# Optimization experiments

Hardware: AMD Instinct MI355X
Metric: run time of the kernel (lower is better)

## Reference

```python
import jax, jax.numpy as jnp
import numpy as np
from jax import lax

ITERATIONS = 10
B, I, D, J, E = 512, 7, 512, 64, 128


def setup_inputs() -> dict:
    key = jax.random.key(0)
    k1, k2, k3 = jax.random.split(key, 3)
    f_bid = jax.random.normal(k1, (B, I, D), dtype=jnp.float32)
    p_bi = jax.random.uniform(k2, (B, I), dtype=jnp.float32)
    weights = jax.random.normal(k3, (I, D, J, E), dtype=jnp.float32)
    return {"f_bid": f_bid, "p_bi": p_bi, "weights": weights}


def reference(f_bid, p_bi, weights):
    # Precompute the per-capsule vote tensor once: [B, I, J, E]
    f_W_bije = jnp.einsum('bid,idje->bije', f_bid, weights)
    b = f_bid.shape[0]
    j, e = weights.shape[2], weights.shape[3]
    c0 = jnp.ones((b, j, e), dtype=f_bid.dtype)

    def body(c_bj, _):
        # routing logits over output capsules j, softmax over j (dim=-1 of 'bij')
        r_bij = jax.nn.softmax(jnp.einsum('bije,bje->bij', f_W_bije, c_bj), axis=-1)
        c_next = jnp.einsum('bi,bij,bije->bje', p_bi, r_bij, f_W_bije)
        return c_next, r_bij

    c_bj, r_stack = lax.scan(body, c0, None, length=ITERATIONS)
    return c_bj, r_stack[-1]
```

## Files before the change

### kernel.cpp

```cpp
#include <hip/hip_runtime.h>
#include <hip/hip_bf16.h>

#define B_SZ 512
#define I_SZ 7
#define D_SZ 512
#define J_SZ 64
#define E_SZ 128
#define N_SZ 8192
#define ITERS 10

typedef __attribute__((ext_vector_type(8))) short bf16x8;
typedef __attribute__((ext_vector_type(4))) float f32x4;

#if defined(__has_builtin)
#if __has_builtin(__builtin_amdgcn_cvt_pk_bf16_f32)
#define HAVE_CVT_PK_BF16 1
#endif
#endif

__device__ inline void split2(float x0, float x1, unsigned& hp, unsigned& lp) {
#ifdef HAVE_CVT_PK_BF16
    auto h = __builtin_amdgcn_cvt_pk_bf16_f32(x0, x1);
    hp = __builtin_bit_cast(unsigned, h);
    union { unsigned u; float f; } b0, b1;
    b0.u = hp << 16;
    b1.u = hp & 0xFFFF0000u;
    auto l = __builtin_amdgcn_cvt_pk_bf16_f32(x0 - b0.f, x1 - b1.f);
    lp = __builtin_bit_cast(unsigned, l);
#else
    union { float f; unsigned u; } u0, u1;
    u0.f = x0; u1.f = x1;
    unsigned r0 = u0.u + 0x7FFF + ((u0.u >> 16) & 1);
    unsigned r1 = u1.u + 0x7FFF + ((u1.u >> 16) & 1);
    hp = __builtin_amdgcn_perm(r1, r0, 0x07060302);
    union { unsigned u; float f; } h0, h1;
    h0.u = r0 & 0xFFFF0000u;
    h1.u = r1 & 0xFFFF0000u;
    union { float f; unsigned u; } s0, s1;
    s0.f = x0 - h0.f; s1.f = x1 - h1.f;
    unsigned q0 = s0.u + 0x7FFF + ((s0.u >> 16) & 1);
    unsigned q1 = s1.u + 0x7FFF + ((s1.u >> 16) & 1);
    lp = __builtin_amdgcn_perm(q1, q0, 0x07060302);
#endif
}

__device__ inline void gload16(const float* g, float* l) {
    __builtin_amdgcn_global_load_lds(
        (const __attribute__((address_space(1))) void*)g,
        (__attribute__((address_space(3))) void*)l, 16, 0, 0);
}

__global__ __launch_bounds__(512) void vote_gemm_mfma(
    const float* __restrict__ f,
    const float* __restrict__ W,
    float* __restrict__ fW)
{
    const int i  = blockIdx.z;
    const int m0 = blockIdx.y * 256;
    const int n0 = blockIdx.x * 256;
    const int th = threadIdx.x;
    const int lane = th & 63;
    const int wave = th >> 6;
    const int wr  = wave >> 2;
    const int wc  = wave & 3;
    const int q   = lane >> 4;
    const int l15 = lane & 15;

    __shared__ float ldsA[2][256 * 32];
    __shared__ float ldsB[2][32 * 256];

    const float* aSrc[4];
    const float* bSrc[4];
#pragma unroll
    for (int ci = 0; ci < 4; ++ci) {
        const int ia = ci * 512 + th;
        const int mA = ia >> 3, sA = ia & 7;
        aSrc[ci] = f + (size_t)(m0 + mA) * (I_SZ * D_SZ) + (size_t)i * D_SZ
                     + ((sA ^ (mA & 7)) << 2);
        const int ib = ci * 512 + th;
        const int kB = ib >> 6, cB = ib & 63;
        bSrc[ci] = W + (size_t)i * D_SZ * N_SZ + (size_t)kB * N_SZ + n0
                     + ((cB ^ ((kB & 8) >> 1)) << 2);
    }

    auto stage = [&](int slot) {
#pragma unroll
        for (int ci = 0; ci < 4; ++ci)
            gload16(aSrc[ci], &ldsA[slot][(ci * 512 + th) * 4]);
#pragma unroll
        for (int ci = 0; ci < 4; ++ci)
            gload16(bSrc[ci], &ldsB[slot][(ci * 512 + th) * 4]);
#pragma unroll
        for (int ci = 0; ci < 4; ++ci) {
            aSrc[ci] += 32;
            bSrc[ci] += (size_t)32 * N_SZ;
        }
    };

    f32x4 acc[8][4];
#pragma unroll
    for (int a = 0; a < 8; ++a)
#pragma unroll
        for (int c = 0; c < 4; ++c)
            acc[a][c] = (f32x4){0.f, 0.f, 0.f, 0.f};

    stage(0);
    stage(1);
    asm volatile("s_waitcnt vmcnt(8)" ::: "memory");
    __builtin_amdgcn_s_barrier();
    asm volatile("" ::: "memory");

    for (int t = 0; t < 16; ++t) {
        const int slot = t & 1;
        const float* Ab = &ldsA[slot][0];
        const float* Bb = &ldsB[slot][0];

        uint4 Bh4[4], Bl4[4];
#pragma unroll
        for (int ns = 0; ns < 4; ++ns) {
            const int cs = (wc * 16 + ns * 4 + (l15 >> 2)) ^ ((q & 1) << 2);
            const float* bp = Bb + q * 8 * 256 + cs * 4 + (l15 & 3);
            const float b0 = bp[0 * 256], b1 = bp[1 * 256], b2 = bp[2 * 256], b3 = bp[3 * 256];
            const float b4 = bp[4 * 256], b5 = bp[5 * 256], b6 = bp[6 * 256], b7 = bp[7 * 256];
            split2(b0, b1, Bh4[ns].x, Bl4[ns].x);
            split2(b2, b3, Bh4[ns].y, Bl4[ns].y);
            split2(b4, b5, Bh4[ns].z, Bl4[ns].z);
            split2(b6, b7, Bh4[ns].w, Bl4[ns].w);
        }

#pragma unroll
        for (int ms = 0; ms < 8; ++ms) {
            const int mrow = wr * 128 + ms * 16 + l15;
            const int p0 = (q * 2) ^ (l15 & 7);
            const float4 va = *(const float4*)(Ab + mrow * 32 + ((p0 ^ 0) << 2));
            const float4 vb = *(const float4*)(Ab + mrow * 32 + ((p0 ^ 1) << 2));
            uint4 ah, al;
            split2(va.x, va.y, ah.x, al.x);
            split2(va.z, va.w, ah.y, al.y);
            split2(vb.x, vb.y, ah.z, al.z);
            split2(vb.z, vb.w, ah.w, al.w);
            const bf16x8 Ah = __builtin_bit_cast(bf16x8, ah);
            const bf16x8 Al = __builtin_bit_cast(bf16x8, al);
            __builtin_amdgcn_s_setprio(1);
#pragma unroll
            for (int ns = 0; ns < 4; ++ns) {
                const bf16x8 Bh = __builtin_bit_cast(bf16x8, Bh4[ns]);
                const bf16x8 Bl = __builtin_bit_cast(bf16x8, Bl4[ns]);
                acc[ms][ns] = __builtin_amdgcn_mfma_f32_16x16x32_bf16(Ah, Bh, acc[ms][ns], 0, 0, 0);
                acc[ms][ns] = __builtin_amdgcn_mfma_f32_16x16x32_bf16(Ah, Bl, acc[ms][ns], 0, 0, 0);
                acc[ms][ns] = __builtin_amdgcn_mfma_f32_16x16x32_bf16(Al, Bh, acc[ms][ns], 0, 0, 0);
            }
            __builtin_amdgcn_s_setprio(0);
        }

        asm volatile("s_waitcnt lgkmcnt(0)" ::: "memory");
        __builtin_amdgcn_s_barrier();
        asm volatile("" ::: "memory");
        if (t < 14) {
            stage(slot);
            asm volatile("s_waitcnt vmcnt(8)" ::: "memory");
        } else {
            asm volatile("s_waitcnt vmcnt(0)" ::: "memory");
        }
        __builtin_amdgcn_s_barrier();
        asm volatile("" ::: "memory");
    }

#pragma unroll
    for (int ms = 0; ms < 8; ++ms) {
        const int rowb = m0 + wr * 128 + ms * 16 + q * 4;
#pragma unroll
        for (int ns = 0; ns < 4; ++ns) {
            const int col = n0 + wc * 64 + ns * 16 + l15;
#pragma unroll
            for (int r = 0; r < 4; ++r)
                fW[((size_t)(rowb + r) * I_SZ + i) * N_SZ + col] = acc[ms][ns][r];
        }
    }
}

__global__ __launch_bounds__(1024) void routing_kernel(
    const float* __restrict__ fW,
    const float* __restrict__ p,
    float* __restrict__ c_out,
    float* __restrict__ r_out)
{
    const int b   = blockIdx.x;
    const int tid = threadIdx.x;
    const int j   = tid >> 4;
    const int sub = tid & 15;

    __shared__ float G_sh[64][49];
    __shared__ float s_sh[64][9];
    __shared__ float w_sh[2][64][9];
    __shared__ float p_sh[8];

    if (tid < I_SZ) p_sh[tid] = p[(size_t)b * I_SZ + tid];

    float4 fw[I_SZ][2];
    const float* base = fW + (size_t)b * I_SZ * N_SZ + j * E_SZ + sub * 8;
#pragma unroll
    for (int i = 0; i < I_SZ; ++i) {
        fw[i][0] = *(const float4*)(base + (size_t)i * N_SZ);
        fw[i][1] = *(const float4*)(base + (size_t)i * N_SZ + 4);
    }

#pragma unroll
    for (int i = 0; i < I_SZ; ++i) {
        float s = fw[i][0].x + fw[i][0].y + fw[i][0].z + fw[i][0].w
                + fw[i][1].x + fw[i][1].y + fw[i][1].z + fw[i][1].w;
        s += __shfl_xor(s, 1); s += __shfl_xor(s, 2);
        s += __shfl_xor(s, 4); s += __shfl_xor(s, 8);
        if (sub == 0) s_sh[j][i] = s;
#pragma unroll
        for (int i2 = i; i2 < I_SZ; ++i2) {
            float g = fw[i][0].x * fw[i2][0].x + fw[i][0].y * fw[i2][0].y
                    + fw[i][0].z * fw[i2][0].z + fw[i][0].w * fw[i2][0].w
                    + fw[i][1].x * fw[i2][1].x + fw[i][1].y * fw[i2][1].y
                    + fw[i][1].z * fw[i2][1].z + fw[i][1].w * fw[i2][1].w;
            g += __shfl_xor(g, 1); g += __shfl_xor(g, 2);
            g += __shfl_xor(g, 4); g += __shfl_xor(g, 8);
            if (sub == 0) { G_sh[j][i * 7 + i2] = g; G_sh[j][i2 * 7 + i] = g; }
        }
    }
    __syncthreads();

    for (int t = 0; t < ITERS; ++t) {
        if (tid < I_SZ * 64) {
            const int ii = tid >> 6;
            const int jj = tid & 63;
            float l;
            if (t == 0) {
                l = s_sh[jj][ii];
            } else {
                const int rb = t & 1;
                l = 0.f;
#pragma unroll
                for (int i2 = 0; i2 < I_SZ; ++i2)
                    l = fmaf(w_sh[rb][jj][i2], G_sh[jj][ii * 7 + i2], l);
            }
            float mx = l;
#pragma unroll
            for (int off = 32; off > 0; off >>= 1)
                mx = fmaxf(mx, __shfl_xor(mx, off));
            float ex = __expf(l - mx);
            float sm = ex;
#pragma unroll
            for (int off = 32; off > 0; off >>= 1)
                sm += __shfl_xor(sm, off);
            float r = ex / sm;
            if (t == ITERS - 1)
                r_out[(size_t)b * (I_SZ * J_SZ) + ii * 64 + jj] = r;
            w_sh[(t + 1) & 1][jj][ii] = p_sh[ii] * r;
        }
        __syncthreads();
    }

    float4 a0 = make_float4(0.f, 0.f, 0.f, 0.f);
    float4 a1 = make_float4(0.f, 0.f, 0.f, 0.f);
#pragma unroll
    for (int i = 0; i < I_SZ; ++i) {
        float wv = w_sh[ITERS & 1][j][i];
        a0.x = fmaf(wv, fw[i][0].x, a0.x); a0.y = fmaf(wv, fw[i][0].y, a0.y);
        a0.z = fmaf(wv, fw[i][0].z, a0.z); a0.w = fmaf(wv, fw[i][0].w, a0.w);
        a1.x = fmaf(wv, fw[i][1].x, a1.x); a1.y = fmaf(wv, fw[i][1].y, a1.y);
        a1.z = fmaf(wv, fw[i][1].z, a1.z); a1.w = fmaf(wv, fw[i][1].w, a1.w);
    }
    float* dst = c_out + (size_t)b * N_SZ + j * E_SZ + sub * 8;
    *(float4*)(dst)     = a0;
    *(float4*)(dst + 4) = a1;
}

extern "C" void kernel_launch(void* const* d_in, const int* in_sizes, int n_in,
                              void* d_out, int out_size, void* d_ws, size_t ws_size,
                              hipStream_t stream) {
    const float* f = (const float*)d_in[0];
    const float* p = (const float*)d_in[1];
    const float* W = (const float*)d_in[2];
    float* out = (float*)d_out;
    float* fW  = (float*)d_ws;

    vote_gemm_mfma<<<dim3(N_SZ / 256, B_SZ / 256, I_SZ), 512, 0, stream>>>(f, W, fW);
    routing_kernel<<<B_SZ, 1024, 0, stream>>>(fW, p, out, out + (size_t)B_SZ * N_SZ);
}
```

Measured before the change: 347.1 us.

## Pre-split GEMM operands to bf16 hi/lo in LDS with register-staged prefetch

The vote GEMM's staging is rewritten so each thread loads the next K-tile from global memory into registers, splits it once into bf16 hi/lo halves, and writes those to swizzled LDS buffers. This replaces the old global_load_lds path, where every wave re-split fp32 values read from LDS. The aim is to remove repeated split work per wave and let the MFMA loop read ready bf16x8 fragments directly, overlapping the next tile's global loads and LDS writes with the MFMAs. It uses more registers for the staged values and adds an occupancy hint of 2 blocks per CU. B is now fetched with strided scalar loads, which may coalesce poorly.

```diff
diff --git a/kernel.cpp b/kernel.cpp
--- a/kernel.cpp
+++ b/kernel.cpp
@@ -44,13 +44,7 @@
 #endif
 }
 
-__device__ inline void gload16(const float* g, float* l) {
-    __builtin_amdgcn_global_load_lds(
-        (const __attribute__((address_space(1))) void*)g,
-        (__attribute__((address_space(3))) void*)l, 16, 0, 0);
-}
-
-__global__ __launch_bounds__(512) void vote_gemm_mfma(
+__global__ __launch_bounds__(512, 2) void vote_gemm_mfma(
     const float* __restrict__ f,
     const float* __restrict__ W,
     float* __restrict__ fW)
@@ -61,41 +55,26 @@
     const int th = threadIdx.x;
     const int lane = th & 63;
     const int wave = th >> 6;
-    const int wr  = wave >> 2;
-    const int wc  = wave & 3;
-    const int q   = lane >> 4;
-    const int l15 = lane & 15;
-
-    __shared__ float ldsA[2][256 * 32];
-    __shared__ float ldsB[2][32 * 256];
-
-    const float* aSrc[4];
-    const float* bSrc[4];
-#pragma unroll
-    for (int ci = 0; ci < 4; ++ci) {
-        const int ia = ci * 512 + th;
-        const int mA = ia >> 3, sA = ia & 7;
-        aSrc[ci] = f + (size_t)(m0 + mA) * (I_SZ * D_SZ) + (size_t)i * D_SZ
-                     + ((sA ^ (mA & 7)) << 2);
-        const int ib = ci * 512 + th;
-        const int kB = ib >> 6, cB = ib & 63;
-        bSrc[ci] = W + (size_t)i * D_SZ * N_SZ + (size_t)kB * N_SZ + n0
-                     + ((cB ^ ((kB & 8) >> 1)) << 2);
-    }
-
-    auto stage = [&](int slot) {
-#pragma unroll
-        for (int ci = 0; ci < 4; ++ci)
-            gload16(aSrc[ci], &ldsA[slot][(ci * 512 + th) * 4]);
-#pragma unroll
-        for (int ci = 0; ci < 4; ++ci)
-            gload16(bSrc[ci], &ldsB[slot][(ci * 512 + th) * 4]);
-#pragma unroll
-        for (int ci = 0; ci < 4; ++ci) {
-            aSrc[ci] += 32;
-            bSrc[ci] += (size_t)32 * N_SZ;
-        }
-    };
+    const int wr   = wave >> 2;
+    const int wc   = wave & 3;
+    const int quad = lane >> 4;
+    const int lm   = lane & 15;
+
+    __shared__ short Ah_s[2][256 * 32];
+    __shared__ short Al_s[2][256 * 32];
+    __shared__ short Bh_s[2][256 * 32];
+    __shared__ short Bl_s[2][256 * 32];
+
+    const int sm = th >> 1;
+    const int kh = th & 1;
+    const int swzw = ((sm & 1) << 1) | ((sm >> 1) & 1);
+    const int wo0 = sm * 32 + (((kh << 1) | 0) ^ swzw) * 8;
+    const int wo1 = sm * 32 + (((kh << 1) | 1) ^ swzw) * 8;
+
+    const float* aPtr = f + (size_t)(m0 + sm) * (I_SZ * D_SZ) + (size_t)i * D_SZ + kh * 16;
+    const float* bPtr = W + (size_t)i * D_SZ * N_SZ + (size_t)(kh * 16) * N_SZ + n0 + sm;
+
+    const int fpos8 = (quad ^ (((lm & 1) << 1) | ((lm >> 1) & 1))) * 8;
 
     f32x4 acc[8][4];
 #pragma unroll
@@ -104,74 +83,102 @@
         for (int c = 0; c < 4; ++c)
             acc[a][c] = (f32x4){0.f, 0.f, 0.f, 0.f};
 
-    stage(0);
-    stage(1);
-    asm volatile("s_waitcnt vmcnt(8)" ::: "memory");
-    __builtin_amdgcn_s_barrier();
-    asm volatile("" ::: "memory");
+    float av[16], bv[16];
+    auto stage_load = [&](int kt) {
+        const float* pa = aPtr + kt * 32;
+        float4 t0 = *(const float4*)(pa);
+        float4 t1 = *(const float4*)(pa + 4);
+        float4 t2 = *(const float4*)(pa + 8);
+        float4 t3 = *(const float4*)(pa + 12);
+        av[0]=t0.x;  av[1]=t0.y;  av[2]=t0.z;  av[3]=t0.w;
+        av[4]=t1.x;  av[5]=t1.y;  av[6]=t1.z;  av[7]=t1.w;
+        av[8]=t2.x;  av[9]=t2.y;  av[10]=t2.z; av[11]=t2.w;
+        av[12]=t3.x; av[13]=t3.y; av[14]=t3.z; av[15]=t3.w;
+        const float* pb = bPtr + (size_t)kt * 32 * N_SZ;
+#pragma unroll
+        for (int r = 0; r < 16; ++r) bv[r] = pb[(size_t)r * N_SZ];
+    };
+    auto stage_write = [&](int slot) {
+        short* qAh = &Ah_s[slot][0]; short* qAl = &Al_s[slot][0];
+        short* qBh = &Bh_s[slot][0]; short* qBl = &Bl_s[slot][0];
+        uint4 h, l;
+        split2(av[0],  av[1],  h.x, l.x); split2(av[2],  av[3],  h.y, l.y);
+        split2(av[4],  av[5],  h.z, l.z); split2(av[6],  av[7],  h.w, l.w);
+        *(uint4*)&qAh[wo0] = h; *(uint4*)&qAl[wo0] = l;
+        split2(av[8],  av[9],  h.x, l.x); split2(av[10], av[11], h.y, l.y);
+        split2(av[12], av[13], h.z, l.z); split2(av[14], av[15], h.w, l.w);
+        *(uint4*)&qAh[wo1] = h; *(uint4*)&qAl[wo1] = l;
+        split2(bv[0],  bv[1],  h.x, l.x); split2(bv[2],  bv[3],  h.y, l.y);
+        split2(bv[4],  bv[5],  h.z, l.z); split2(bv[6],  bv[7],  h.w, l.w);
+        *(uint4*)&qBh[wo0] = h; *(uint4*)&qBl[wo0] = l;
+        split2(bv[8],  bv[9],  h.x, l.x); split2(bv[10], bv[11], h.y, l.y);
+        split2(bv[12], bv[13], h.z, l.z); split2(bv[14], bv[15], h.w, l.w);
+        *(uint4*)&qBh[wo1] = h; *(uint4*)&qBl[wo1] = l;
+    };
+
+    stage_load(0);
+    stage_write(0);
+    __syncthreads();
 
     for (int t = 0; t < 16; ++t) {
-        const int slot = t & 1;
-        const float* Ab = &ldsA[slot][0];
-        const float* Bb = &ldsB[slot][0];
-
-        uint4 Bh4[4], Bl4[4];
+        const int s = t & 1;
+        const short* pAh = &Ah_s[s][0]; const short* pAl = &Al_s[s][0];
+        const short* pBh = &Bh_s[s][0]; const short* pBl = &Bl_s[s][0];
+
+        if (t < 15) stage_load(t + 1);
+        __builtin_amdgcn_sched_barrier(0);
+
+        bf16x8 Bf_h[4], Bf_l[4];
 #pragma unroll
         for (int ns = 0; ns < 4; ++ns) {
-            const int cs = (wc * 16 + ns * 4 + (l15 >> 2)) ^ ((q & 1) << 2);
-            const float* bp = Bb + q * 8 * 256 + cs * 4 + (l15 & 3);
-            const float b0 = bp[0 * 256], b1 = bp[1 * 256], b2 = bp[2 * 256], b3 = bp[3 * 256];
-            const float b4 = bp[4 * 256], b5 = bp[5 * 256], b6 = bp[6 * 256], b7 = bp[7 * 256];
-            split2(b0, b1, Bh4[ns].x, Bl4[ns].x);
-            split2(b2, b3, Bh4[ns].y, Bl4[ns].y);
-            split2(b4, b5, Bh4[ns].z, Bl4[ns].z);
-            split2(b6, b7, Bh4[ns].w, Bl4[ns].w);
-        }
-
-#pragma unroll
-        for (int ms = 0; ms < 8; ++ms) {
-            const int mrow = wr * 128 + ms * 16 + l15;
-            const int p0 = (q * 2) ^ (l15 & 7);
-            const float4 va = *(const float4*)(Ab + mrow * 32 + ((p0 ^ 0) << 2));
-            const float4 vb = *(const float4*)(Ab + mrow * 32 + ((p0 ^ 1) << 2));
-            uint4 ah, al;
-            split2(va.x, va.y, ah.x, al.x);
-            split2(va.z, va.w, ah.y, al.y);
-            split2(vb.x, vb.y, ah.z, al.z);
-            split2(vb.z, vb.w, ah.w, al.w);
-            const bf16x8 Ah = __builtin_bit_cast(bf16x8, ah);
-            const bf16x8 Al = __builtin_bit_cast(bf16x8, al);
+            const int o = (wc * 64 + ns * 16 + lm) * 32 + fpos8;
+            Bf_h[ns] = *(const bf16x8*)&pBh[o];
+            Bf_l[ns] = *(const bf16x8*)&pBl[o];
+        }
+#pragma unroll
+        for (int ms = 0; ms < 6; ++ms) {
+            const int o = (wr * 128 + ms * 16 + lm) * 32 + fpos8;
+            const bf16x8 Af_h = *(const bf16x8*)&pAh[o];
+            const bf16x8 Af_l = *(const bf16x8*)&pAl[o];
             __builtin_amdgcn_s_setprio(1);
 #pragma unroll
             for (int ns = 0; ns < 4; ++ns) {
-                const bf16x8 Bh = __builtin_bit_cast(bf16x8, Bh4[ns]);
-                const bf16x8 Bl = __builtin_bit_cast(bf16x8, Bl4[ns]);
-                acc[ms][ns] = __builtin_amdgcn_mfma_f32_16x16x32_bf16(Ah, Bh, acc[ms][ns], 0, 0, 0);
-                acc[ms][ns] = __builtin_amdgcn_mfma_f32_16x16x32_bf16(Ah, Bl, acc[ms][ns], 0, 0, 0);
-                acc[ms][ns] = __builtin_amdgcn_mfma_f32_16x16x32_bf16(Al, Bh, acc[ms][ns], 0, 0, 0);
+                acc[ms][ns] = __builtin_amdgcn_mfma_f32_16x16x32_bf16(Af_h, Bf_h[ns], acc[ms][ns], 0, 0, 0);
+                acc[ms][ns] = __builtin_amdgcn_mfma_f32_16x16x32_bf16(Af_h, Bf_l[ns], acc[ms][ns], 0, 0, 0);
+                acc[ms][ns] = __builtin_amdgcn_mfma_f32_16x16x32_bf16(Af_l, Bf_h[ns], acc[ms][ns], 0, 0, 0);
             }
             __builtin_amdgcn_s_setprio(0);
         }
-
-        asm volatile("s_waitcnt lgkmcnt(0)" ::: "memory");
-        __builtin_amdgcn_s_barrier();
-        asm volatile("" ::: "memory");
-        if (t < 14) {
-            stage(slot);
-            asm volatile("s_waitcnt vmcnt(8)" ::: "memory");
-        } else {
-            asm volatile("s_waitcnt vmcnt(0)" ::: "memory");
-        }
-        __builtin_amdgcn_s_barrier();
-        asm volatile("" ::: "memory");
+        __builtin_amdgcn_sched_barrier(0);
+
+        if (t < 15) stage_write(s ^ 1);
+        __builtin_amdgcn_sched_barrier(0);
+
+#pragma unroll
+        for (int ms = 6; ms < 8; ++ms) {
+            const int o = (wr * 128 + ms * 16 + lm) * 32 + fpos8;
+            const bf16x8 Af_h = *(const bf16x8*)&pAh[o];
+            const bf16x8 Af_l = *(const bf16x8*)&pAl[o];
+            __builtin_amdgcn_s_setprio(1);
+#pragma unroll
+            for (int ns = 0; ns < 4; ++ns) {
+                acc[ms][ns] = __builtin_amdgcn_mfma_f32_16x16x32_bf16(Af_h, Bf_h[ns], acc[ms][ns], 0, 0, 0);
+                acc[ms][ns] = __builtin_amdgcn_mfma_f32_16x16x32_bf16(Af_h, Bf_l[ns], acc[ms][ns], 0, 0, 0);
+                acc[ms][ns] = __builtin_amdgcn_mfma_f32_16x16x32_bf16(Af_l, Bf_h[ns], acc[ms][ns], 0, 0, 0);
+            }
+            __builtin_amdgcn_s_setprio(0);
+        }
+        __builtin_amdgcn_sched_barrier(0);
+
+        __syncthreads();
     }
 
 #pragma unroll
     for (int ms = 0; ms < 8; ++ms) {
-        const int rowb = m0 + wr * 128 + ms * 16 + q * 4;
+        const int rowb = m0 + wr * 128 + ms * 16 + quad * 4;
 #pragma unroll
         for (int ns = 0; ns < 4; ++ns) {
-            const int col = n0 + wc * 64 + ns * 16 + l15;
+            const int col = n0 + wc * 64 + ns * 16 + lm;
 #pragma unroll
             for (int r = 0; r < 4; ++r)
                 fW[((size_t)(rowb + r) * I_SZ + i) * N_SZ + col] = acc[ms][ns][r];
```

Result: faster. 309.2 us (-10.9%).
